# Kernel optimization log

Hardware: AMD Instinct MI355X
Metric: run time of the kernel (lower is better)

## Reference

```python
import jax, jax.numpy as jnp
import numpy as np

BETA = 0.25


def setup_inputs() -> dict:
    key = jax.random.key(0)
    k1, k2, k3 = jax.random.split(key, 3)
    B, C, D, H, W = 2, 256, 16, 56, 56
    K = 1024
    z = jax.random.normal(k1, (B, C, D, H, W), dtype=jnp.float32)
    # Embedding init: uniform(-1/K, 1/K)
    key_weight = jax.random.uniform(k2, (K, C), dtype=jnp.float32, minval=-1.0 / K, maxval=1.0 / K)
    value_weight = jax.random.uniform(k3, (K, C), dtype=jnp.float32, minval=-1.0 / K, maxval=1.0 / K)
    return {"z": z, "key_weight": key_weight, "value_weight": value_weight}


def reference(z, key_weight, value_weight):
    # z: [B, C, D, H, W] -> [B, D, H, W, C]
    zp = jnp.transpose(z, (0, 2, 3, 4, 1))
    B, D, H, W, C = zp.shape
    z_flat = zp.reshape(-1, C)  # [N, C]
    # Squared euclidean distances to codebook: ||z||^2 + ||e||^2 - 2 z e^T
    d = (jnp.sum(z_flat ** 2, axis=1, keepdims=True)
         + jnp.sum(key_weight ** 2, axis=1)
         - 2.0 * jnp.matmul(z_flat, key_weight.T))  # [N, K]
    idx = jnp.argmin(d, axis=1)  # [N]
    z_q_key = key_weight[idx].reshape(zp.shape)    # [B, D, H, W, C]
    z_q_value = value_weight[idx].reshape(zp.shape)
    sg = jax.lax.stop_gradient
    loss = jnp.mean((sg(z_q_key) - zp) ** 2) + BETA * jnp.mean((z_q_key - sg(zp)) ** 2)
    z_q_value = jnp.transpose(z_q_value, (0, 4, 1, 2, 3))  # [B, C, D, H, W]
    return z_q_value, idx, loss
```

## Files before the change

kernel.cpp:

```cpp
#include <hip/hip_runtime.h>
#include <stdint.h>

constexpr int Cc   = 256;
constexpr int Kc   = 1024;
constexpr int NLOC = 16 * 56 * 56;
constexpr int NB   = 2;
constexpr int NTOT = NB * NLOC;
constexpr long long ZQV = (long long)NB * Cc * NLOC;

constexpr int SR   = 128;
constexpr int SC   = 128;
constexpr int BK   = 64;
constexpr int NCH  = Cc / BK;
constexpr int NRT  = NTOT / SR;
constexpr int NSL  = Kc / SC;
constexpr int SBLK = NRT * NSL;

constexpr int   SLOTS = 16;
constexpr float WIN   = 3e-4f;
constexpr float NEG2S = -0.001953125f;

constexpr int F1B = NTOT / 256;
constexpr int RB  = 32;
constexpr int F2B = NTOT / RB;
constexpr int DSB = NTOT / 256;

using f16x8 = __attribute__((ext_vector_type(8))) _Float16;
using f32x4 = __attribute__((ext_vector_type(4))) float;
typedef unsigned long long u64;
typedef unsigned int       u32;
typedef unsigned short     u16;

__device__ __forceinline__ float sqf(float x) {
    float s = x * x;
    asm("" : "+v"(s));
    return s;
}

template <typename Loader>
__device__ __forceinline__ float pw256_sq(Loader ld)
{
    float half[2];
    #pragma unroll
    for (int h = 0; h < 2; ++h) {
        float r[8];
        #pragma unroll
        for (int j = 0; j < 8; ++j) r[j] = sqf(ld(h * 128 + j));
        #pragma unroll
        for (int i = 8; i < 128; i += 8)
            #pragma unroll
            for (int j = 0; j < 8; ++j) r[j] += sqf(ld(h * 128 + i + j));
        half[h] = ((r[0] + r[1]) + (r[2] + r[3])) + ((r[4] + r[5]) + (r[6] + r[7]));
    }
    return half[0] + half[1];
}

__global__ void esq_pw(const float* __restrict__ key, float* __restrict__ esq)
{
    int k = blockIdx.x * 256 + threadIdx.x;
    if (k < Kc) {
        const float* a = key + (size_t)k * Cc;
        esq[k] = pw256_sq([&](int c) { return a[c]; });
    }
}

__device__ __forceinline__ u16 f16b(float x)
{
    _Float16 h = (_Float16)x;
    u16 r;
    __builtin_memcpy(&r, &h, 2);
    return r;
}

__global__ void split_e(const float* __restrict__ key, u16* __restrict__ ef16)
{
    int i = blockIdx.x * 256 + threadIdx.x;
    if (i < Kc * Cc) ef16[i] = f16b(key[i] * 1024.0f);
}

__global__ __launch_bounds__(256, 2)
void split_z(const float* __restrict__ z, u16* __restrict__ zf16,
             float* __restrict__ zt32, float* __restrict__ zsq)
{
    __shared__ float t[64][260];
    const int tid = threadIdx.x;
    const int n0  = blockIdx.x * 64;
    const int b   = (n0 >= NLOC) ? 1 : 0;
    const int loc0 = n0 - b * NLOC;
    const float* zb = z + (size_t)b * Cc * NLOC;

    {
        const int n4 = tid & 15;
        #pragma unroll
        for (int it = 0; it < 4; ++it) {
            int c4 = (tid >> 4) + it * 16;
            float4 g0 = *reinterpret_cast<const float4*>(zb + (size_t)(c4 * 4 + 0) * NLOC + loc0 + n4 * 4);
            float4 g1 = *reinterpret_cast<const float4*>(zb + (size_t)(c4 * 4 + 1) * NLOC + loc0 + n4 * 4);
            float4 g2 = *reinterpret_cast<const float4*>(zb + (size_t)(c4 * 4 + 2) * NLOC + loc0 + n4 * 4);
            float4 g3 = *reinterpret_cast<const float4*>(zb + (size_t)(c4 * 4 + 3) * NLOC + loc0 + n4 * 4);
            *reinterpret_cast<float4*>(&t[n4 * 4 + 0][c4 * 4]) = make_float4(g0.x, g1.x, g2.x, g3.x);
            *reinterpret_cast<float4*>(&t[n4 * 4 + 1][c4 * 4]) = make_float4(g0.y, g1.y, g2.y, g3.y);
            *reinterpret_cast<float4*>(&t[n4 * 4 + 2][c4 * 4]) = make_float4(g0.z, g1.z, g2.z, g3.z);
            *reinterpret_cast<float4*>(&t[n4 * 4 + 3][c4 * 4]) = make_float4(g0.w, g1.w, g2.w, g3.w);
        }
    }
    __syncthreads();
    {
        const int row2 = tid >> 5;
        const int ch   = tid & 31;
        #pragma unroll
        for (int rg = 0; rg < 8; ++rg) {
            int row = rg * 8 + row2;
            float4 f0 = *reinterpret_cast<const float4*>(&t[row][ch * 8]);
            float4 f1 = *reinterpret_cast<const float4*>(&t[row][ch * 8 + 4]);
            float xs[8] = {f0.x, f0.y, f0.z, f0.w, f1.x, f1.y, f1.z, f1.w};
            u32 hp[4];
            #pragma unroll
            for (int j = 0; j < 4; ++j)
                hp[j] = (u32)f16b(xs[2 * j]) | ((u32)f16b(xs[2 * j + 1]) << 16);
            size_t o = ((size_t)(n0 + row)) * Cc + ch * 8;
            *reinterpret_cast<uint4*>(zf16 + o) = make_uint4(hp[0], hp[1], hp[2], hp[3]);
            if (zt32) {
                *reinterpret_cast<float4*>(zt32 + o)     = f0;
                *reinterpret_cast<float4*>(zt32 + o + 4) = f1;
            }
        }
    }
    if (tid < 64)
        zsq[n0 + tid] = pw256_sq([&](int c) { return t[tid][c]; });
}

__device__ __forceinline__ void gload16(const u16* g, u16* lds)
{
    __builtin_amdgcn_global_load_lds(
        (const __attribute__((address_space(1))) u32*)g,
        (__attribute__((address_space(3))) u32*)lds, 16, 0, 0);
}

__global__ __launch_bounds__(256, 4)
void screen(const u16* __restrict__ zf16, const u16* __restrict__ ef16,
            const float* __restrict__ esq, const float* __restrict__ zsq,
            u64* __restrict__ cand, int* __restrict__ cnt)
{
    __shared__ u16  A_lds[SR * BK];
    __shared__ u16  B_lds[SC * BK];
    __shared__ float gm[2][SR];
    __shared__ float esq_s[SC];
    __shared__ float zsq_s[SR];

    const int tid = threadIdx.x;
    const int bid = blockIdx.x;
    const int q   = bid >> 3;
    const int rt  = (bid & 7) * (NRT / 8) + (q >> 3);
    const int r0  = rt * SR;
    const int k0  = (q & 7) * SC;
    const int wid = tid >> 6, l = tid & 63;
    const int wr  = wid >> 1, wc = wid & 1;

    for (int i = tid; i < SC; i += 256) esq_s[i] = esq[k0 + i];
    for (int i = tid; i < SR; i += 256) zsq_s[i] = zsq[r0 + i];

    f32x4 acc[4][4];
    #pragma unroll
    for (int i = 0; i < 4; ++i)
        #pragma unroll
        for (int j = 0; j < 4; ++j)
            acc[i][j] = f32x4{0.f, 0.f, 0.f, 0.f};

    for (int ch = 0; ch < NCH; ++ch) {
        __syncthreads();
        {
            const int lr = l >> 3;
            #pragma unroll
            for (int t = 0; t < 4; ++t) {
                int rowb = wid * 32 + t * 8;
                int row  = rowb + lr;
                int g    = (l & 7) ^ (row & 7);
                gload16(zf16 + (size_t)(r0 + row) * Cc + ch * BK + g * 8,
                        A_lds + rowb * BK);
                gload16(ef16 + (size_t)(k0 + row) * Cc + ch * BK + g * 8,
                        B_lds + rowb * BK);
            }
        }
        __syncthreads();

        #pragma unroll
        for (int kk = 0; kk < 2; ++kk) {
            f16x8 af[4], bf[4];
            const int G = kk * 4 + (l >> 4);
            #pragma unroll
            for (int i = 0; i < 4; ++i) {
                int row = wr * 64 + i * 16 + (l & 15);
                int pg  = G ^ (row & 7);
                af[i] = *reinterpret_cast<const f16x8*>(&A_lds[row * BK + pg * 8]);
            }
            #pragma unroll
            for (int j = 0; j < 4; ++j) {
                int col = wc * 64 + j * 16 + (l & 15);
                int pg  = G ^ (col & 7);
                bf[j] = *reinterpret_cast<const f16x8*>(&B_lds[col * BK + pg * 8]);
            }
            #pragma unroll
            for (int i = 0; i < 4; ++i)
                #pragma unroll
                for (int j = 0; j < 4; ++j)
                    acc[i][j] = __builtin_amdgcn_mfma_f32_16x16x32_f16(
                        af[i], bf[j], acc[i][j], 0, 0, 0);
        }
    }

    #pragma unroll
    for (int i = 0; i < 4; ++i) {
        #pragma unroll
        for (int r = 0; r < 4; ++r) {
            int rloc = wr * 64 + i * 16 + ((l >> 4) << 2) + r;
            float zq = zsq_s[rloc];
            float mn = 3.4e38f;
            #pragma unroll
            for (int j = 0; j < 4; ++j) {
                int cl = wc * 64 + j * 16 + (l & 15);
                float d = fmaf(NEG2S, acc[i][j][r], zq + esq_s[cl]);
                mn = fminf(mn, d);
            }
            #pragma unroll
            for (int m = 1; m < 16; m <<= 1)
                mn = fminf(mn, __shfl_xor(mn, m, 64));
            if ((l & 15) == 0) gm[wc][rloc] = mn;
        }
    }
    __syncthreads();

    #pragma unroll
    for (int i = 0; i < 4; ++i) {
        #pragma unroll
        for (int r = 0; r < 4; ++r) {
            int rloc = wr * 64 + i * 16 + ((l >> 4) << 2) + r;
            float thr = fminf(gm[0][rloc], gm[1][rloc]) + WIN;
            float zq = zsq_s[rloc];
            int rg = r0 + rloc;
            #pragma unroll
            for (int j = 0; j < 4; ++j) {
                int cl = wc * 64 + j * 16 + (l & 15);
                float d = fmaf(NEG2S, acc[i][j][r], zq + esq_s[cl]);
                if (d <= thr) {
                    int slot = atomicAdd(&cnt[rg], 1);
                    if (slot < SLOTS)
                        cand[(size_t)rg * SLOTS + slot] =
                            ((u64)__float_as_uint(d) << 32) | (u32)(k0 + cl);
                }
            }
        }
    }
}

__global__ __launch_bounds__(256)
void resolve_pick(const u64* __restrict__ cand, const int* __restrict__ cnt,
                  int* __restrict__ idxw, float* __restrict__ dbest,
                  float* __restrict__ out,
                  int* __restrict__ wl, int* __restrict__ wcount)
{
    const int p = blockIdx.x * 256 + threadIdx.x;
    const int c = cnt[p];
    const int n = (c < SLOTS) ? c : SLOTS;
    u64 best = 0xFFFFFFFFFFFFFFFFull;
    for (int s = 0; s < n; ++s) {
        u64 v = cand[(size_t)p * SLOTS + s];
        if (v < best) best = v;
    }
    const float db = __uint_as_float((u32)(best >> 32));

    bool needs = (c > SLOTS);
    if (!needs) {
        int namb = 0;
        for (int s = 0; s < n; ++s) {
            float dv = __uint_as_float((u32)(cand[(size_t)p * SLOTS + s] >> 32));
            namb += (dv <= db + WIN) ? 1 : 0;
        }
        needs = (namb > 1);
    }
    if (needs) wl[atomicAdd(wcount, 1)] = p;

    idxw[p] = (int)(u32)best;
    dbest[p] = db;
    out[ZQV + p] = (float)(u32)best;
}

__global__ __launch_bounds__(256)
void rescore(const float* __restrict__ zt32, const float* __restrict__ key,
             const float* __restrict__ esq, const float* __restrict__ zsq,
             const u64* __restrict__ cand, const int* __restrict__ cnt,
             const int* __restrict__ wcount, const int* __restrict__ wl,
             int* __restrict__ idxw, float* __restrict__ dbest,
             float* __restrict__ out)
{
    const int i = blockIdx.x * 256 + threadIdx.x;
    if (i >= *wcount) return;
    const int p = wl[i];
    const float* zr = zt32 + (size_t)p * Cc;
    const float zq = zsq[p];
    const int c = cnt[p];
    u64 bb = 0xFFFFFFFFFFFFFFFFull;

    if (c > SLOTS) {
        for (int k = 0; k < Kc; ++k) {
            const float* kr = key + (size_t)k * Cc;
            float m = 0.f;
            for (int cc = 0; cc < Cc; ++cc)
                m = fmaf(zr[cc], kr[cc], m);
            float d = fmaf(-2.0f, m, zq + esq[k]);
            u64 pk = ((u64)__float_as_uint(d) << 32) | (u32)k;
            if (pk < bb) bb = pk;
        }
    } else {
        u64 best = 0xFFFFFFFFFFFFFFFFull;
        for (int s = 0; s < c; ++s) {
            u64 v = cand[(size_t)p * SLOTS + s];
            if (v < best) best = v;
        }
        const float db = __uint_as_float((u32)(best >> 32));
        for (int s = 0; s < c; ++s) {
            u64 v = cand[(size_t)p * SLOTS + s];
            float dv = __uint_as_float((u32)(v >> 32));
            if (dv <= db + WIN) {
                int k = (int)(u32)v;
                const float* kr = key + (size_t)k * Cc;
                float m = 0.f;
                for (int cc = 0; cc < Cc; ++cc)
                    m = fmaf(zr[cc], kr[cc], m);
                float d = fmaf(-2.0f, m, zq + esq[k]);
                u64 pk = ((u64)__float_as_uint(d) << 32) | (u32)k;
                if (pk < bb) bb = pk;
            }
        }
    }
    idxw[p] = (int)(u32)bb;
    dbest[p] = __uint_as_float((u32)(bb >> 32));
    out[ZQV + p] = (float)(u32)bb;
}

__global__ __launch_bounds__(256)
void resolve_fallback(const float* __restrict__ z, const float* __restrict__ key,
                      const float* __restrict__ esq, const float* __restrict__ zsq,
                      const u64* __restrict__ cand, const int* __restrict__ cnt,
                      float* __restrict__ out, int* __restrict__ idxw,
                      float* __restrict__ dbest)
{
    const int p   = blockIdx.x * 256 + threadIdx.x;
    const int b   = (p >= NLOC) ? 1 : 0;
    const int loc = p - b * NLOC;
    const float* zb = z + (size_t)b * Cc * NLOC;

    const int c = cnt[p];
    const int n = (c < SLOTS) ? c : SLOTS;
    u64 best = 0xFFFFFFFFFFFFFFFFull;
    for (int s = 0; s < n; ++s) {
        u64 v = cand[(size_t)p * SLOTS + s];
        if (v < best) best = v;
    }
    u64 sel = best;
    const float db = __uint_as_float((u32)(best >> 32));

    if (c > SLOTS) {
        u64 bb = 0xFFFFFFFFFFFFFFFFull;
        for (int k = 0; k < Kc; ++k) {
            const float* kr = key + (size_t)k * Cc;
            float m = 0.f;
            for (int cc = 0; cc < Cc; ++cc)
                m = fmaf(zb[(size_t)cc * NLOC + loc], kr[cc], m);
            float d = fmaf(-2.0f, m, zsq[p] + esq[k]);
            u64 pk = ((u64)__float_as_uint(d) << 32) | (u32)k;
            if (pk < bb) bb = pk;
        }
        sel = bb;
    } else {
        int namb = 0;
        for (int s = 0; s < n; ++s) {
            float dv = __uint_as_float((u32)(cand[(size_t)p * SLOTS + s] >> 32));
            namb += (dv <= db + WIN) ? 1 : 0;
        }
        if (namb > 1) {
            u64 bb = 0xFFFFFFFFFFFFFFFFull;
            for (int s = 0; s < n; ++s) {
                u64 v = cand[(size_t)p * SLOTS + s];
                float dv = __uint_as_float((u32)(v >> 32));
                if (dv <= db + WIN) {
                    int k = (int)(u32)v;
                    const float* kr = key + (size_t)k * Cc;
                    float m = 0.f;
                    for (int cc = 0; cc < Cc; ++cc)
                        m = fmaf(zb[(size_t)cc * NLOC + loc], kr[cc], m);
                    float d = fmaf(-2.0f, m, zsq[p] + esq[k]);
                    u64 pk = ((u64)__float_as_uint(d) << 32) | (u32)k;
                    if (pk < bb) bb = pk;
                }
            }
            sel = bb;
        }
    }
    idxw[p] = (int)(u32)sel;
    dbest[p] = __uint_as_float((u32)(sel >> 32));
    out[ZQV + p] = (float)(u32)sel;
}

__global__ __launch_bounds__(256)
void gather(const float* __restrict__ val, const int* __restrict__ idxw,
            float* __restrict__ out)
{
    __shared__ float rowbuf[RB][261];
    __shared__ int   idx_sh[RB];
    const int tid = threadIdx.x, blk = blockIdx.x;
    const int wid = tid >> 6, l = tid & 63;
    const int p0  = blk * RB;
    const int b   = (p0 >= NLOC) ? 1 : 0;
    const int loc0 = p0 - b * NLOC;

    if (tid < RB) idx_sh[tid] = idxw[p0 + tid];
    __syncthreads();

    #pragma unroll
    for (int i = 0; i < RB / 4; ++i) {
        int row = wid * (RB / 4) + i;
        float4 v = *reinterpret_cast<const float4*>(val + (size_t)idx_sh[row] * Cc + l * 4);
        *reinterpret_cast<float4*>(&rowbuf[row][l * 4]) = v;
    }
    __syncthreads();

    const int nq = l & 7;
    #pragma unroll
    for (int it = 0; it < 8; ++it) {
        int cc = (l >> 3) + 8 * it + 64 * wid;
        float4 v = make_float4(rowbuf[nq * 4 + 0][cc], rowbuf[nq * 4 + 1][cc],
                               rowbuf[nq * 4 + 2][cc], rowbuf[nq * 4 + 3][cc]);
        *reinterpret_cast<float4*>(
            out + ((size_t)b * Cc + cc) * NLOC + loc0 + nq * 4) = v;
    }
}

__global__ __launch_bounds__(256)
void dsum(const float* __restrict__ dbest, double* __restrict__ partial)
{
    __shared__ double wred[4];
    const int tid = threadIdx.x;
    double s = (double)dbest[blockIdx.x * 256 + tid];
    for (int off = 32; off > 0; off >>= 1) s += __shfl_down(s, off);
    if ((tid & 63) == 0) wred[tid >> 6] = s;
    __syncthreads();
    if (tid == 0) partial[blockIdx.x] = wred[0] + wred[1] + wred[2] + wred[3];
}

__global__ void fin_kernel(const double* __restrict__ partial, float* __restrict__ out_loss)
{
    __shared__ double sh[256];
    double s = 0.0;
    for (int i = threadIdx.x; i < DSB; i += 256) s += partial[i];
    sh[threadIdx.x] = s;
    __syncthreads();
    for (int st = 128; st > 0; st >>= 1) {
        if (threadIdx.x < st) sh[threadIdx.x] += sh[threadIdx.x + st];
        __syncthreads();
    }
    if (threadIdx.x == 0)
        out_loss[0] = (float)(1.25 * sh[0] / (double)((long long)NTOT * Cc));
}

extern "C" void kernel_launch(void* const* d_in, const int* in_sizes, int n_in,
                              void* d_out, int out_size, void* d_ws, size_t ws_size,
                              hipStream_t stream)
{
    const float* z   = (const float*)d_in[0];
    const float* key = (const float*)d_in[1];
    const float* val = (const float*)d_in[2];
    float* out = (float*)d_out;

    u16* zf16 = (u16*)d_out;

    char* w = (char*)d_ws;
    u16*    ef16    = (u16*)w;                 w += (size_t)Kc * Cc * 2;
    u64*    cand    = (u64*)w;                 w += (size_t)NTOT * SLOTS * 8;
    int*    cnt     = (int*)w;                 w += (size_t)NTOT * 4;
    int*    wcount  = (int*)w;                 w += 16;
    int*    idxw    = (int*)w;                 w += (size_t)NTOT * 4;
    int*    wl      = (int*)w;                 w += (size_t)NTOT * 4;
    float*  dbest   = (float*)w;               w += (size_t)NTOT * 4;
    double* partial = (double*)w;              w += (size_t)DSB * 8;
    float*  esq     = (float*)w;               w += (size_t)Kc * 4;
    float*  zsq     = (float*)w;               w += (size_t)NTOT * 4;
    float*  zt32    = (float*)w;
    size_t  need_big = (size_t)(w - (char*)d_ws) + (size_t)NTOT * Cc * 4;
    const bool big = ws_size >= need_big;

    hipMemsetAsync(cnt, 0, (size_t)NTOT * 4 + 16, stream);
    hipLaunchKernelGGL(esq_pw, dim3((Kc + 255) / 256), dim3(256), 0, stream, key, esq);
    hipLaunchKernelGGL(split_e, dim3((Kc * Cc + 255) / 256), dim3(256), 0, stream, key, ef16);
    hipLaunchKernelGGL(split_z, dim3(NTOT / 64), dim3(256), 0, stream, z, zf16,
                       big ? zt32 : (float*)nullptr, zsq);
    hipLaunchKernelGGL(screen, dim3(SBLK), dim3(256), 0, stream,
                       zf16, ef16, esq, zsq, cand, cnt);
    if (big) {
        hipLaunchKernelGGL(resolve_pick, dim3(F1B), dim3(256), 0, stream,
                           cand, cnt, idxw, dbest, out, wl, wcount);
        hipLaunchKernelGGL(rescore, dim3(F1B), dim3(256), 0, stream,
                           zt32, key, esq, zsq, cand, cnt, wcount, wl, idxw, dbest, out);
    } else {
        hipLaunchKernelGGL(resolve_fallback, dim3(F1B), dim3(256), 0, stream,
                           z, key, esq, zsq, cand, cnt, out, idxw, dbest);
    }
    hipLaunchKernelGGL(gather, dim3(F2B), dim3(256), 0, stream, val, idxw, out);
    hipLaunchKernelGGL(dsum, dim3(DSB), dim3(256), 0, stream, dbest, partial);
    hipLaunchKernelGGL(fin_kernel, dim3(1), dim3(256), 0, stream, partial, out + ZQV + NTOT);
}
```

Before: 378.6 us.

## Fuse small prep kernels, halve split_z LDS, fold loss partials into gather

Merges the memset, esq_pw and split_e launches into a single prep_key kernel, and folds the dsum reduction into the gather kernel so each gather block writes its own partial. split_z now handles the channels in two halves through a 64x132 LDS tile, which cuts shared memory per block and lets launch bounds allow 4 blocks per CU. This targets launch overhead and split_z occupancy, at the cost of an extra barrier in split_z, more partials for fin_kernel to sum, and esq being computed by only the first 1024 threads of a large grid.

```diff
diff --git a/kernel.cpp b/kernel.cpp
--- a/kernel.cpp
+++ b/kernel.cpp
@@ -23,7 +23,6 @@
 constexpr int F1B = NTOT / 256;
 constexpr int RB  = 32;
 constexpr int F2B = NTOT / RB;
-constexpr int DSB = NTOT / 256;
 
 using f16x8 = __attribute__((ext_vector_type(8))) _Float16;
 using f32x4 = __attribute__((ext_vector_type(4))) float;
@@ -38,30 +37,24 @@
 }
 
 template <typename Loader>
+__device__ __forceinline__ float pw128_sq(Loader ld)
+{
+    float r[8];
+    #pragma unroll
+    for (int j = 0; j < 8; ++j) r[j] = sqf(ld(j));
+    #pragma unroll
+    for (int i = 8; i < 128; i += 8)
+        #pragma unroll
+        for (int j = 0; j < 8; ++j) r[j] += sqf(ld(i + j));
+    return ((r[0] + r[1]) + (r[2] + r[3])) + ((r[4] + r[5]) + (r[6] + r[7]));
+}
+
+template <typename Loader>
 __device__ __forceinline__ float pw256_sq(Loader ld)
 {
-    float half[2];
-    #pragma unroll
-    for (int h = 0; h < 2; ++h) {
-        float r[8];
-        #pragma unroll
-        for (int j = 0; j < 8; ++j) r[j] = sqf(ld(h * 128 + j));
-        #pragma unroll
-        for (int i = 8; i < 128; i += 8)
-            #pragma unroll
-            for (int j = 0; j < 8; ++j) r[j] += sqf(ld(h * 128 + i + j));
-        half[h] = ((r[0] + r[1]) + (r[2] + r[3])) + ((r[4] + r[5]) + (r[6] + r[7]));
-    }
-    return half[0] + half[1];
-}
-
-__global__ void esq_pw(const float* __restrict__ key, float* __restrict__ esq)
-{
-    int k = blockIdx.x * 256 + threadIdx.x;
-    if (k < Kc) {
-        const float* a = key + (size_t)k * Cc;
-        esq[k] = pw256_sq([&](int c) { return a[c]; });
-    }
+    float h0 = pw128_sq([&](int c) { return ld(c); });
+    float h1 = pw128_sq([&](int c) { return ld(128 + c); });
+    return h0 + h1;
 }
 
 __device__ __forceinline__ u16 f16b(float x)
@@ -72,62 +65,80 @@
     return r;
 }
 
-__global__ void split_e(const float* __restrict__ key, u16* __restrict__ ef16)
+__global__ void prep_key(const float* __restrict__ key, u16* __restrict__ ef16,
+                         float* __restrict__ esq,
+                         int* __restrict__ cnt, int* __restrict__ wcount)
 {
     int i = blockIdx.x * 256 + threadIdx.x;
     if (i < Kc * Cc) ef16[i] = f16b(key[i] * 1024.0f);
-}
-
-__global__ __launch_bounds__(256, 2)
+    if (i < NTOT) cnt[i] = 0;
+    if (i == 0) *wcount = 0;
+    if (i < Kc) {
+        const float* a = key + (size_t)i * Cc;
+        esq[i] = pw256_sq([&](int c) { return a[c]; });
+    }
+}
+
+__global__ __launch_bounds__(256, 4)
 void split_z(const float* __restrict__ z, u16* __restrict__ zf16,
              float* __restrict__ zt32, float* __restrict__ zsq)
 {
-    __shared__ float t[64][260];
+    __shared__ float t[64][132];
     const int tid = threadIdx.x;
     const int n0  = blockIdx.x * 64;
     const int b   = (n0 >= NLOC) ? 1 : 0;
     const int loc0 = n0 - b * NLOC;
     const float* zb = z + (size_t)b * Cc * NLOC;
 
-    {
-        const int n4 = tid & 15;
-        #pragma unroll
-        for (int it = 0; it < 4; ++it) {
-            int c4 = (tid >> 4) + it * 16;
-            float4 g0 = *reinterpret_cast<const float4*>(zb + (size_t)(c4 * 4 + 0) * NLOC + loc0 + n4 * 4);
-            float4 g1 = *reinterpret_cast<const float4*>(zb + (size_t)(c4 * 4 + 1) * NLOC + loc0 + n4 * 4);
-            float4 g2 = *reinterpret_cast<const float4*>(zb + (size_t)(c4 * 4 + 2) * NLOC + loc0 + n4 * 4);
-            float4 g3 = *reinterpret_cast<const float4*>(zb + (size_t)(c4 * 4 + 3) * NLOC + loc0 + n4 * 4);
-            *reinterpret_cast<float4*>(&t[n4 * 4 + 0][c4 * 4]) = make_float4(g0.x, g1.x, g2.x, g3.x);
-            *reinterpret_cast<float4*>(&t[n4 * 4 + 1][c4 * 4]) = make_float4(g0.y, g1.y, g2.y, g3.y);
-            *reinterpret_cast<float4*>(&t[n4 * 4 + 2][c4 * 4]) = make_float4(g0.z, g1.z, g2.z, g3.z);
-            *reinterpret_cast<float4*>(&t[n4 * 4 + 3][c4 * 4]) = make_float4(g0.w, g1.w, g2.w, g3.w);
-        }
-    }
-    __syncthreads();
-    {
-        const int row2 = tid >> 5;
-        const int ch   = tid & 31;
-        #pragma unroll
-        for (int rg = 0; rg < 8; ++rg) {
-            int row = rg * 8 + row2;
-            float4 f0 = *reinterpret_cast<const float4*>(&t[row][ch * 8]);
-            float4 f1 = *reinterpret_cast<const float4*>(&t[row][ch * 8 + 4]);
-            float xs[8] = {f0.x, f0.y, f0.z, f0.w, f1.x, f1.y, f1.z, f1.w};
-            u32 hp[4];
-            #pragma unroll
-            for (int j = 0; j < 4; ++j)
-                hp[j] = (u32)f16b(xs[2 * j]) | ((u32)f16b(xs[2 * j + 1]) << 16);
-            size_t o = ((size_t)(n0 + row)) * Cc + ch * 8;
-            *reinterpret_cast<uint4*>(zf16 + o) = make_uint4(hp[0], hp[1], hp[2], hp[3]);
-            if (zt32) {
-                *reinterpret_cast<float4*>(zt32 + o)     = f0;
-                *reinterpret_cast<float4*>(zt32 + o + 4) = f1;
-            }
-        }
-    }
-    if (tid < 64)
-        zsq[n0 + tid] = pw256_sq([&](int c) { return t[tid][c]; });
+    float hs0 = 0.f;
+
+    #pragma unroll
+    for (int h = 0; h < 2; ++h) {
+        if (h) __syncthreads();
+        {
+            const int n4 = tid & 15;
+            #pragma unroll
+            for (int it = 0; it < 2; ++it) {
+                int c4 = (tid >> 4) + it * 16;
+                int cg = h * 128 + c4 * 4;
+                float4 g0 = *reinterpret_cast<const float4*>(zb + (size_t)(cg + 0) * NLOC + loc0 + n4 * 4);
+                float4 g1 = *reinterpret_cast<const float4*>(zb + (size_t)(cg + 1) * NLOC + loc0 + n4 * 4);
+                float4 g2 = *reinterpret_cast<const float4*>(zb + (size_t)(cg + 2) * NLOC + loc0 + n4 * 4);
+                float4 g3 = *reinterpret_cast<const float4*>(zb + (size_t)(cg + 3) * NLOC + loc0 + n4 * 4);
+                *reinterpret_cast<float4*>(&t[n4 * 4 + 0][c4 * 4]) = make_float4(g0.x, g1.x, g2.x, g3.x);
+                *reinterpret_cast<float4*>(&t[n4 * 4 + 1][c4 * 4]) = make_float4(g0.y, g1.y, g2.y, g3.y);
+                *reinterpret_cast<float4*>(&t[n4 * 4 + 2][c4 * 4]) = make_float4(g0.z, g1.z, g2.z, g3.z);
+                *reinterpret_cast<float4*>(&t[n4 * 4 + 3][c4 * 4]) = make_float4(g0.w, g1.w, g2.w, g3.w);
+            }
+        }
+        __syncthreads();
+        {
+            const int row2 = tid >> 4;
+            const int ch   = tid & 15;
+            #pragma unroll
+            for (int rg = 0; rg < 4; ++rg) {
+                int row = rg * 16 + row2;
+                float4 f0 = *reinterpret_cast<const float4*>(&t[row][ch * 8]);
+                float4 f1 = *reinterpret_cast<const float4*>(&t[row][ch * 8 + 4]);
+                float xs[8] = {f0.x, f0.y, f0.z, f0.w, f1.x, f1.y, f1.z, f1.w};
+                u32 hp[4];
+                #pragma unroll
+                for (int j = 0; j < 4; ++j)
+                    hp[j] = (u32)f16b(xs[2 * j]) | ((u32)f16b(xs[2 * j + 1]) << 16);
+                size_t o = ((size_t)(n0 + row)) * Cc + h * 128 + ch * 8;
+                *reinterpret_cast<uint4*>(zf16 + o) = make_uint4(hp[0], hp[1], hp[2], hp[3]);
+                if (zt32) {
+                    *reinterpret_cast<float4*>(zt32 + o)     = f0;
+                    *reinterpret_cast<float4*>(zt32 + o + 4) = f1;
+                }
+            }
+        }
+        if (tid < 64) {
+            float hv = pw128_sq([&](int c) { return t[tid][c]; });
+            if (h == 0) hs0 = hv;
+            else        zsq[n0 + tid] = hs0 + hv;
+        }
+    }
 }
 
 __device__ __forceinline__ void gload16(const u16* g, u16* lds)
@@ -404,7 +415,8 @@
 
 __global__ __launch_bounds__(256)
 void gather(const float* __restrict__ val, const int* __restrict__ idxw,
-            float* __restrict__ out)
+            const float* __restrict__ dbest,
+            float* __restrict__ out, double* __restrict__ partial)
 {
     __shared__ float rowbuf[RB][261];
     __shared__ int   idx_sh[RB];
@@ -415,6 +427,12 @@
     const int loc0 = p0 - b * NLOC;
 
     if (tid < RB) idx_sh[tid] = idxw[p0 + tid];
+
+    if (tid < 64) {
+        double s = (tid < RB) ? (double)dbest[p0 + tid] : 0.0;
+        for (int off = 32; off > 0; off >>= 1) s += __shfl_down(s, off);
+        if (tid == 0) partial[blk] = s;
+    }
     __syncthreads();
 
     #pragma unroll
@@ -436,23 +454,11 @@
     }
 }
 
-__global__ __launch_bounds__(256)
-void dsum(const float* __restrict__ dbest, double* __restrict__ partial)
-{
-    __shared__ double wred[4];
-    const int tid = threadIdx.x;
-    double s = (double)dbest[blockIdx.x * 256 + tid];
-    for (int off = 32; off > 0; off >>= 1) s += __shfl_down(s, off);
-    if ((tid & 63) == 0) wred[tid >> 6] = s;
-    __syncthreads();
-    if (tid == 0) partial[blockIdx.x] = wred[0] + wred[1] + wred[2] + wred[3];
-}
-
 __global__ void fin_kernel(const double* __restrict__ partial, float* __restrict__ out_loss)
 {
     __shared__ double sh[256];
     double s = 0.0;
-    for (int i = threadIdx.x; i < DSB; i += 256) s += partial[i];
+    for (int i = threadIdx.x; i < F2B; i += 256) s += partial[i];
     sh[threadIdx.x] = s;
     __syncthreads();
     for (int st = 128; st > 0; st >>= 1) {
@@ -482,16 +488,15 @@
     int*    idxw    = (int*)w;                 w += (size_t)NTOT * 4;
     int*    wl      = (int*)w;                 w += (size_t)NTOT * 4;
     float*  dbest   = (float*)w;               w += (size_t)NTOT * 4;
-    double* partial = (double*)w;              w += (size_t)DSB * 8;
+    double* partial = (double*)w;              w += (size_t)F2B * 8;
     float*  esq     = (float*)w;               w += (size_t)Kc * 4;
     float*  zsq     = (float*)w;               w += (size_t)NTOT * 4;
     float*  zt32    = (float*)w;
     size_t  need_big = (size_t)(w - (char*)d_ws) + (size_t)NTOT * Cc * 4;
     const bool big = ws_size >= need_big;
 
-    hipMemsetAsync(cnt, 0, (size_t)NTOT * 4 + 16, stream);
-    hipLaunchKernelGGL(esq_pw, dim3((Kc + 255) / 256), dim3(256), 0, stream, key, esq);
-    hipLaunchKernelGGL(split_e, dim3((Kc * Cc + 255) / 256), dim3(256), 0, stream, key, ef16);
+    hipLaunchKernelGGL(prep_key, dim3((Kc * Cc + 255) / 256), dim3(256), 0, stream,
+                       key, ef16, esq, cnt, wcount);
     hipLaunchKernelGGL(split_z, dim3(NTOT / 64), dim3(256), 0, stream, z, zf16,
                        big ? zt32 : (float*)nullptr, zsq);
     hipLaunchKernelGGL(screen, dim3(SBLK), dim3(256), 0, stream,
@@ -505,7 +510,7 @@
         hipLaunchKernelGGL(resolve_fallback, dim3(F1B), dim3(256), 0, stream,
                            z, key, esq, zsq, cand, cnt, out, idxw, dbest);
     }
-    hipLaunchKernelGGL(gather, dim3(F2B), dim3(256), 0, stream, val, idxw, out);
-    hipLaunchKernelGGL(dsum, dim3(DSB), dim3(256), 0, stream, dbest, partial);
+    hipLaunchKernelGGL(gather, dim3(F2B), dim3(256), 0, stream,
+                       val, idxw, dbest, out, partial);
     hipLaunchKernelGGL(fin_kernel, dim3(1), dim3(256), 0, stream, partial, out + ZQV + NTOT);
 }
```

New measurement: 376.1 us. About the same (-0.7%).
